# Optimization experiments

Measured on AMD Instinct MI355X. Metric: run time of the kernel, lower is better.

Reference implementation:

```python
import jax, jax.numpy as jnp
import numpy as np

N_QUBITS = 8
N_LAYERS = 4


def _apply_1q(state, U, q):
    """Apply a 2x2 gate U (shape (2,2) shared, or (B,2,2) per-sample) on qubit q.
    state: (B, 2, 2, ..., 2) with qubit q on axis q+1 (wire 0 = most significant)."""
    a = q + 1
    st = jnp.moveaxis(state, a, -1)
    shp = st.shape
    st = st.reshape(shp[0], -1, 2)  # (B, rest, 2)
    if U.ndim == 3:
        st = jnp.einsum('bij,brj->bri', U, st)
    else:
        st = jnp.einsum('ij,brj->bri', U, st)
    return jnp.moveaxis(st.reshape(shp), -1, a)


def _cnot(state, c, t):
    ac, at = c + 1, t + 1
    s0 = jnp.take(state, 0, axis=ac)
    s1 = jnp.take(state, 1, axis=ac)
    at2 = at - 1 if at > ac else at  # axis shift after removing control axis
    s1 = jnp.flip(s1, axis=at2)      # X on target where control = 1
    return jnp.stack([s0, s1], axis=ac)


def _rx(t):
    c = jnp.cos(t / 2)
    s = jnp.sin(t / 2)
    return jnp.stack([jnp.stack([c + 0j, -1j * s]),
                      jnp.stack([-1j * s, c + 0j])]).astype(jnp.complex64)


def _ry(t):
    c = jnp.cos(t / 2)
    s = jnp.sin(t / 2)
    return jnp.stack([jnp.stack([c, -s]),
                      jnp.stack([s, c])]).astype(jnp.complex64)


def _rz(t):
    return jnp.diag(jnp.stack([jnp.exp(-1j * t / 2),
                               jnp.exp(1j * t / 2)])).astype(jnp.complex64)


def _ry_batched(t):
    # t: (B,) -> (B, 2, 2)
    c = jnp.cos(t / 2)
    s = jnp.sin(t / 2)
    U = jnp.stack([jnp.stack([c, -s], axis=-1),
                   jnp.stack([s, c], axis=-1)], axis=-2)
    return U.astype(jnp.complex64)


def setup_inputs() -> dict:
    key = jax.random.key(0)
    k1, k2 = jax.random.split(key)
    B = 16384
    x = jax.random.normal(k1, (B, N_QUBITS), dtype=jnp.float32)
    weights = jax.random.normal(k2, (N_QUBITS * N_LAYERS * 3,), dtype=jnp.float32) * 0.1
    return {"x": x, "weights": weights}


def reference(x, weights):
    n, L = N_QUBITS, N_LAYERS
    B = x.shape[0]
    state = jnp.zeros((B,) + (2,) * n, dtype=jnp.complex64)
    state = state.at[(slice(None),) + (0,) * n].set(1.0)

    # angle encoding: per-sample RY on each wire
    for q in range(n):
        state = _apply_1q(state, _ry_batched(x[:, q]), q)

    idx = 0
    for _ in range(L):
        for q in range(n):
            state = _apply_1q(state, _rx(weights[idx]), q)
            state = _apply_1q(state, _ry(weights[idx + 1]), q)
            state = _apply_1q(state, _rz(weights[idx + 2]), q)
            idx += 3
        for q in range(n - 1):
            state = _cnot(state, q, q + 1)

    p = jnp.abs(state) ** 2  # (B, 2, ..., 2) float32
    outs = []
    for q in range(n):
        axes = tuple(a for a in range(1, n + 1) if a != q + 1)
        z = p.sum(axis=axes)  # (B, 2)
        outs.append(z[:, 0] - z[:, 1])
    return jnp.stack(outs, axis=-1).astype(jnp.float32)
```

## Files before the change

### kernel.cpp

```cpp
#include <hip/hip_runtime.h>


#define NGATES 32

constexpr bool selon(int l, int d) {
    return (l == 0) ? (d == 0) : (((d + l - 1) & (l - 1)) == (l - 1));
}
constexpr int lm_of(int l, int q) {
    int m = 0;
    for (int d = 0; q + d <= 7; ++d)
        if ((l & d) == d) { int qq = q + d; if (qq <= 3) m |= 1 << (3 - qq); }
    return m;
}
constexpr int rm_of(int l, int q) {
    int m = 0;
    for (int d = 0; q + d <= 7; ++d)
        if ((l & d) == d) { int qq = q + d; if (qq >= 4) m |= 1 << (7 - qq); }
    return m;
}
constexpr int slm_of(int l, int q) {
    int m = 0;
    for (int d = 0; d <= q; ++d)
        if (selon(l, d)) { int k = q - d; if (k <= 3) m |= 1 << (3 - k); }
    return m;
}
constexpr int srm_of(int l, int q) {
    int m = 0;
    for (int d = 0; d <= q; ++d)
        if (selon(l, d)) { int k = q - d; if (k >= 4) m |= 1 << (7 - k); }
    return m;
}

__device__ __forceinline__ float xsgn(float f, unsigned m) {
    return __int_as_float(__float_as_int(f) ^ (int)m);
}

template<int C>
__device__ __forceinline__ int dppmov(int x) {
    return __builtin_amdgcn_update_dpp(x, x, C, 0xF, 0xF, false);
}

template<int M>
__device__ __forceinline__ float shx(float v) {
    static_assert(M >= 1 && M <= 15, "xor mask out of range");
    int x = __float_as_int(v);
    if constexpr (M == 1)       { x = dppmov<0xB1>(x); }
    else if constexpr (M == 2)  { x = dppmov<0x4E>(x); }
    else if constexpr (M == 3)  { x = dppmov<0x1B>(x); }
    else if constexpr (M == 4)  { x = dppmov<0x1B>(x);  x = dppmov<0x141>(x); }
    else if constexpr (M == 5)  { x = dppmov<0x4E>(x);  x = dppmov<0x141>(x); }
    else if constexpr (M == 6)  { x = dppmov<0xB1>(x);  x = dppmov<0x141>(x); }
    else if constexpr (M == 7)  { x = dppmov<0x141>(x); }
    else if constexpr (M == 8)  { x = dppmov<0x128>(x); }
    else if constexpr (M == 9)  { x = dppmov<0xB1>(x);  x = dppmov<0x128>(x); }
    else if constexpr (M == 10) { x = dppmov<0x4E>(x);  x = dppmov<0x128>(x); }
    else if constexpr (M == 11) { x = dppmov<0x1B>(x);  x = dppmov<0x128>(x); }
    else if constexpr (M == 12) { x = dppmov<0x140>(x); x = dppmov<0x1B>(x);  }
    else if constexpr (M == 13) { x = dppmov<0x140>(x); x = dppmov<0x4E>(x);  }
    else if constexpr (M == 14) { x = dppmov<0x140>(x); x = dppmov<0xB1>(x);  }
    else                        { x = dppmov<0x140>(x); }
    return __int_as_float(x);
}

template<int LM, int RM, int SLM, int SRM>
__device__ __forceinline__ void apply_gate(float ar[16], float ai[16], int lane,
                                           const float4 g)
{
    unsigned sm = 0;
    if constexpr (SLM != 0)
        sm = (unsigned)((__builtin_popcount(lane & SLM) & 1) << 31);
    const float c0r = g.x, c1i = g.w;
    const float c0i0 = xsgn(g.y, sm);
    const float c1r0 = xsgn(g.z, sm);
    const float c0i1 = xsgn(g.y, sm ^ 0x80000000u);
    const float c1r1 = xsgn(g.z, sm ^ 0x80000000u);

    if constexpr (RM == 0) {
        #pragma unroll
        for (int r = 0; r < 16; ++r) {
            const bool c1 = (__builtin_popcount(r & SRM) & 1) != 0;
            const float c0i = c1 ? c0i1 : c0i0;
            const float c1r = c1 ? c1r1 : c1r0;
            const float br = shx<LM>(ar[r]);
            const float bi = shx<LM>(ai[r]);
            const float nr = c0r*ar[r] - c0i*ai[r] + c1r*br - c1i*bi;
            const float ni = c0r*ai[r] + c0i*ar[r] + c1r*bi + c1i*br;
            ar[r] = nr; ai[r] = ni;
        }
    } else {
        #pragma unroll
        for (int r = 0; r < 16; ++r) {
            const int p = r ^ RM;
            if (p < r) continue;
            float br_r, bi_r, br_p, bi_p;
            if constexpr (LM != 0) {
                br_r = shx<LM>(ar[p]); bi_r = shx<LM>(ai[p]);
                br_p = shx<LM>(ar[r]); bi_p = shx<LM>(ai[r]);
            } else {
                br_r = ar[p]; bi_r = ai[p];
                br_p = ar[r]; bi_p = ai[r];
            }
            const bool cr = (__builtin_popcount(r & SRM) & 1) != 0;
            const bool cp = (__builtin_popcount(p & SRM) & 1) != 0;
            const float c0i_r = cr ? c0i1 : c0i0, c1r_r = cr ? c1r1 : c1r0;
            const float c0i_p = cp ? c0i1 : c0i0, c1r_p = cp ? c1r1 : c1r0;
            const float nr_r = c0r*ar[r] - c0i_r*ai[r] + c1r_r*br_r - c1i*bi_r;
            const float ni_r = c0r*ai[r] + c0i_r*ar[r] + c1r_r*bi_r + c1i*br_r;
            const float nr_p = c0r*ar[p] - c0i_p*ai[p] + c1r_p*br_p - c1i*bi_p;
            const float ni_p = c0r*ai[p] + c0i_p*ar[p] + c1r_p*bi_p + c1i*br_p;
            ar[r] = nr_r; ai[r] = ni_r;
            ar[p] = nr_p; ai[p] = ni_p;
        }
    }
}

#define GATE(L, Q) apply_gate<lm_of(L,Q), rm_of(L,Q), slm_of(L,Q), srm_of(L,Q)>( \
                       ar, ai, lane, gsh4[(L)*8+(Q)])
#define LAYER(L) GATE(L,0); GATE(L,1); GATE(L,2); GATE(L,3); \
                 GATE(L,4); GATE(L,5); GATE(L,6); GATE(L,7);

__global__ __launch_bounds__(256, 4) void qsim(const float* __restrict__ x,
                                               const float* __restrict__ w,
                                               float* __restrict__ out, int B)
{
    __shared__ float4 gsh4[NGATES];

    const int tid = threadIdx.x;
    if (tid < NGATES) {
        float hx = 0.5f * w[tid*3+0];
        float hy = 0.5f * w[tid*3+1];
        float hz = 0.5f * w[tid*3+2];
        float cx = cosf(hx), sx = sinf(hx);
        float cy = cosf(hy), sy = sinf(hy);
        float cz = cosf(hz), sz = sinf(hz);
        float m00r = cy*cx,  m00i =  sy*sx;
        float m01r = -sy*cx, m01i = -cy*sx;
        gsh4[tid] = make_float4(cz*m00r + sz*m00i,
                                cz*m00i - sz*m00r,
                                cz*m01r + sz*m01i,
                                cz*m01i - sz*m01r);
    }
    __syncthreads();

    const int lane = tid & 63;
    const int il   = lane & 15;
    const int sample = blockIdx.x * 16 + (tid >> 4);
    if (sample >= B) return;

    const float4* xp = (const float4*)(x + sample * 8);
    float4 xa = xp[0], xb = xp[1];
    float xs[8] = {xa.x, xa.y, xa.z, xa.w, xb.x, xb.y, xb.z, xb.w};
    float cq[8], sq[8];
    #pragma unroll
    for (int q = 0; q < 8; ++q) {
        float h = 0.5f * xs[q];
        __sincosf(h, &sq[q], &cq[q]);
    }
    float lp = ((il & 8) ? sq[0] : cq[0]);
    lp      *= ((il & 4) ? sq[1] : cq[1]);
    lp      *= ((il & 2) ? sq[2] : cq[2]);
    lp      *= ((il & 1) ? sq[3] : cq[3]);
    float t67[4] = {cq[6]*cq[7], cq[6]*sq[7], sq[6]*cq[7], sq[6]*sq[7]};
    float a5[2]  = {cq[5], sq[5]};
    float a4[2]  = {cq[4]*lp, sq[4]*lp};
    float ar[16], ai[16];
    #pragma unroll
    for (int r = 0; r < 16; ++r) {
        ar[r] = a4[(r >> 3) & 1] * a5[(r >> 2) & 1] * t67[r & 3];
        ai[r] = 0.f;
    }

    LAYER(0)
    LAYER(1)
    LAYER(2)
    LAYER(3)

    float p[16];
    #pragma unroll
    for (int r = 0; r < 16; ++r) p[r] = ar[r]*ar[r] + ai[r]*ai[r];

    float s0[8], d0[8];
    #pragma unroll
    for (int k = 0; k < 8; ++k) { s0[k] = p[2*k] + p[2*k+1]; d0[k] = p[2*k] - p[2*k+1]; }
    float A0 = ((d0[0]+d0[1]) + (d0[2]+d0[3])) + ((d0[4]+d0[5]) + (d0[6]+d0[7]));
    float s1[4], d1[4];
    #pragma unroll
    for (int k = 0; k < 4; ++k) { s1[k] = s0[2*k] + s0[2*k+1]; d1[k] = s0[2*k] - s0[2*k+1]; }
    float A1 = (d1[0]+d1[1]) + (d1[2]+d1[3]);
    float s2[2], d2[2];
    #pragma unroll
    for (int k = 0; k < 2; ++k) { s2[k] = s1[2*k] + s1[2*k+1]; d2[k] = s1[2*k] - s1[2*k+1]; }
    float A2 = d2[0] + d2[1];
    float A3 = s2[0] - s2[1];
    float P  = s2[0] + s2[1];

    const unsigned sg1 = (unsigned)(il & 1) << 31;
    const unsigned sg2 = (unsigned)(il & 2) << 30;
    const unsigned sg4 = (unsigned)(il & 4) << 29;
    const unsigned sg8 = (unsigned)(il & 8) << 28;

    float wP = P;
    { float t = shx<1>(wP); wP = t + xsgn(wP, sg1); }
    { float t = shx<2>(wP); wP = t + xsgn(wP, sg2); }
    { float t = shx<4>(wP); wP = t + xsgn(wP, sg4); }
    { float t = shx<8>(wP); wP = t + xsgn(wP, sg8); }

    float a3 = xsgn(A3, sg8);
    a3 += shx<1>(a3); a3 += shx<2>(a3); a3 += shx<4>(a3); a3 += shx<8>(a3);
    float a2 = xsgn(A2, sg4);
    a2 += shx<1>(a2); a2 += shx<2>(a2); a2 += shx<4>(a2); a2 += shx<8>(a2);
    float a1 = xsgn(A1, sg2);
    a1 += shx<1>(a1); a1 += shx<2>(a1); a1 += shx<4>(a1); a1 += shx<8>(a1);
    float a0 = xsgn(A0, sg1);
    a0 += shx<1>(a0); a0 += shx<2>(a0); a0 += shx<4>(a0); a0 += shx<8>(a0);

    float* op = out + sample * 8;
    if (il == 8)      { op[0] = wP; op[4] = a3; }
    else if (il == 4) { op[1] = wP; op[5] = a2; }
    else if (il == 2) { op[2] = wP; op[6] = a1; }
    else if (il == 1) { op[3] = wP; op[7] = a0; }
}

extern "C" void kernel_launch(void* const* d_in, const int* in_sizes, int n_in,
                              void* d_out, int out_size, void* d_ws, size_t ws_size,
                              hipStream_t stream) {
    const float* x = (const float*)d_in[0];
    const float* w = (const float*)d_in[1];
    float* out = (float*)d_out;
    const int B = in_sizes[0] / 8;
    const int blocks = (B + 15) / 16;
    qsim<<<blocks, 256, 0, stream>>>(x, w, out, B);
}
```

Baseline: 92.70 us.

## Pack complex amplitudes into float2 and use packed FMA with ds_swizzle shuffles

Stores each complex amplitude as a two-float vector and computes each gate update with four packed v_pk_mul/v_pk_fma instructions in inline asm, where the scalar version needed separate real and imaginary FMAs. The intent is to roughly halve VALU instruction count for the gate math. Lane-xor masks that needed two DPP moves now use a single ds_swizzle, which trades VALU work for LDS-pipe latency. The inline asm may also limit compiler scheduling and add register-pair move overhead.

```diff
diff --git a/kernel.cpp b/kernel.cpp
--- a/kernel.cpp
+++ b/kernel.cpp
@@ -2,6 +2,10 @@
 
 
 #define NGATES 32
+
+typedef float v2f __attribute__((ext_vector_type(2)));
+
+__device__ __forceinline__ v2f mk2(float a, float b) { v2f t; t.x = a; t.y = b; return t; }
 
 constexpr bool selon(int l, int d) {
     return (l == 0) ? (d == 0) : (((d + l - 1) & (l - 1)) == (l - 1));
@@ -34,88 +38,90 @@
 __device__ __forceinline__ float xsgn(float f, unsigned m) {
     return __int_as_float(__float_as_int(f) ^ (int)m);
 }
+
 
 template<int C>
 __device__ __forceinline__ int dppmov(int x) {
     return __builtin_amdgcn_update_dpp(x, x, C, 0xF, 0xF, false);
 }
-
 template<int M>
-__device__ __forceinline__ float shx(float v) {
-    static_assert(M >= 1 && M <= 15, "xor mask out of range");
+__device__ __forceinline__ float shx_dpp(float v) {
     int x = __float_as_int(v);
     if constexpr (M == 1)       { x = dppmov<0xB1>(x); }
     else if constexpr (M == 2)  { x = dppmov<0x4E>(x); }
     else if constexpr (M == 3)  { x = dppmov<0x1B>(x); }
-    else if constexpr (M == 4)  { x = dppmov<0x1B>(x);  x = dppmov<0x141>(x); }
-    else if constexpr (M == 5)  { x = dppmov<0x4E>(x);  x = dppmov<0x141>(x); }
-    else if constexpr (M == 6)  { x = dppmov<0xB1>(x);  x = dppmov<0x141>(x); }
     else if constexpr (M == 7)  { x = dppmov<0x141>(x); }
     else if constexpr (M == 8)  { x = dppmov<0x128>(x); }
-    else if constexpr (M == 9)  { x = dppmov<0xB1>(x);  x = dppmov<0x128>(x); }
-    else if constexpr (M == 10) { x = dppmov<0x4E>(x);  x = dppmov<0x128>(x); }
-    else if constexpr (M == 11) { x = dppmov<0x1B>(x);  x = dppmov<0x128>(x); }
-    else if constexpr (M == 12) { x = dppmov<0x140>(x); x = dppmov<0x1B>(x);  }
-    else if constexpr (M == 13) { x = dppmov<0x140>(x); x = dppmov<0x4E>(x);  }
-    else if constexpr (M == 14) { x = dppmov<0x140>(x); x = dppmov<0xB1>(x);  }
     else                        { x = dppmov<0x140>(x); }
     return __int_as_float(x);
 }
+template<int M>
+__device__ __forceinline__ float shx_ds(float v) {
+    return __int_as_float(__builtin_amdgcn_ds_swizzle(__float_as_int(v), (M << 10) | 0x1F));
+}
+constexpr bool sgl(int M) {
+    return M == 1 || M == 2 || M == 3 || M == 7 || M == 8 || M == 15;
+}
+template<int M>
+__device__ __forceinline__ float shxm(float v) {
+    if constexpr (sgl(M)) return shx_dpp<M>(v);
+    else                  return shx_ds<M>(v);
+}
+
+__device__ __forceinline__ v2f cplx4(v2f K0, v2f K1, v2f A, v2f B) {
+    v2f n;
+    asm("v_pk_mul_f32 %0, %1, %2 op_sel:[0,0] op_sel_hi:[0,1]\n\t"
+        "v_pk_fma_f32 %0, %1, %2, %0 op_sel:[1,1,0] op_sel_hi:[1,0,1] neg_lo:[1,0,0]\n\t"
+        "v_pk_fma_f32 %0, %3, %4, %0 op_sel:[0,0,0] op_sel_hi:[0,1,1]\n\t"
+        "v_pk_fma_f32 %0, %3, %4, %0 op_sel:[1,1,0] op_sel_hi:[1,0,1] neg_lo:[1,0,0]"
+        : "=&v"(n)
+        : "v"(K0), "v"(A), "v"(K1), "v"(B));
+    return n;
+}
 
 template<int LM, int RM, int SLM, int SRM>
-__device__ __forceinline__ void apply_gate(float ar[16], float ai[16], int lane,
-                                           const float4 g)
+__device__ __forceinline__ void apply_gate(v2f A[16], int lane, const float4 g)
 {
     unsigned sm = 0;
     if constexpr (SLM != 0)
         sm = (unsigned)((__builtin_popcount(lane & SLM) & 1) << 31);
-    const float c0r = g.x, c1i = g.w;
-    const float c0i0 = xsgn(g.y, sm);
-    const float c1r0 = xsgn(g.z, sm);
-    const float c0i1 = xsgn(g.y, sm ^ 0x80000000u);
-    const float c1r1 = xsgn(g.z, sm ^ 0x80000000u);
+    v2f K0[2], K1[2];
+    K0[0] = mk2(g.x, xsgn(g.y, sm));
+    K0[1] = mk2(g.x, xsgn(g.y, sm ^ 0x80000000u));
+    K1[0] = mk2(xsgn(g.z, sm), g.w);
+    K1[1] = mk2(xsgn(g.z, sm ^ 0x80000000u), g.w);
 
     if constexpr (RM == 0) {
         #pragma unroll
         for (int r = 0; r < 16; ++r) {
-            const bool c1 = (__builtin_popcount(r & SRM) & 1) != 0;
-            const float c0i = c1 ? c0i1 : c0i0;
-            const float c1r = c1 ? c1r1 : c1r0;
-            const float br = shx<LM>(ar[r]);
-            const float bi = shx<LM>(ai[r]);
-            const float nr = c0r*ar[r] - c0i*ai[r] + c1r*br - c1i*bi;
-            const float ni = c0r*ai[r] + c0i*ar[r] + c1r*bi + c1i*br;
-            ar[r] = nr; ai[r] = ni;
+            const int v = __builtin_popcount(r & SRM) & 1;
+            v2f B = mk2(shxm<LM>(A[r].x), shxm<LM>(A[r].y));
+            A[r] = cplx4(K0[v], K1[v], A[r], B);
         }
     } else {
         #pragma unroll
         for (int r = 0; r < 16; ++r) {
             const int p = r ^ RM;
             if (p < r) continue;
-            float br_r, bi_r, br_p, bi_p;
+            v2f Br, Bp;
             if constexpr (LM != 0) {
-                br_r = shx<LM>(ar[p]); bi_r = shx<LM>(ai[p]);
-                br_p = shx<LM>(ar[r]); bi_p = shx<LM>(ai[r]);
+                Br = mk2(shxm<LM>(A[p].x), shxm<LM>(A[p].y));
+                Bp = mk2(shxm<LM>(A[r].x), shxm<LM>(A[r].y));
             } else {
-                br_r = ar[p]; bi_r = ai[p];
-                br_p = ar[r]; bi_p = ai[r];
+                Br = A[p];
+                Bp = A[r];
             }
-            const bool cr = (__builtin_popcount(r & SRM) & 1) != 0;
-            const bool cp = (__builtin_popcount(p & SRM) & 1) != 0;
-            const float c0i_r = cr ? c0i1 : c0i0, c1r_r = cr ? c1r1 : c1r0;
-            const float c0i_p = cp ? c0i1 : c0i0, c1r_p = cp ? c1r1 : c1r0;
-            const float nr_r = c0r*ar[r] - c0i_r*ai[r] + c1r_r*br_r - c1i*bi_r;
-            const float ni_r = c0r*ai[r] + c0i_r*ar[r] + c1r_r*bi_r + c1i*br_r;
-            const float nr_p = c0r*ar[p] - c0i_p*ai[p] + c1r_p*br_p - c1i*bi_p;
-            const float ni_p = c0r*ai[p] + c0i_p*ar[p] + c1r_p*bi_p + c1i*br_p;
-            ar[r] = nr_r; ai[r] = ni_r;
-            ar[p] = nr_p; ai[p] = ni_p;
+            const int vr = __builtin_popcount(r & SRM) & 1;
+            const int vp = __builtin_popcount(p & SRM) & 1;
+            v2f nr = cplx4(K0[vr], K1[vr], A[r], Br);
+            v2f np = cplx4(K0[vp], K1[vp], A[p], Bp);
+            A[r] = nr; A[p] = np;
         }
     }
 }
 
 #define GATE(L, Q) apply_gate<lm_of(L,Q), rm_of(L,Q), slm_of(L,Q), srm_of(L,Q)>( \
-                       ar, ai, lane, gsh4[(L)*8+(Q)])
+                       A, lane, gsh4[(L)*8+(Q)])
 #define LAYER(L) GATE(L,0); GATE(L,1); GATE(L,2); GATE(L,3); \
                  GATE(L,4); GATE(L,5); GATE(L,6); GATE(L,7);
 
@@ -163,12 +169,10 @@
     float t67[4] = {cq[6]*cq[7], cq[6]*sq[7], sq[6]*cq[7], sq[6]*sq[7]};
     float a5[2]  = {cq[5], sq[5]};
     float a4[2]  = {cq[4]*lp, sq[4]*lp};
-    float ar[16], ai[16];
-    #pragma unroll
-    for (int r = 0; r < 16; ++r) {
-        ar[r] = a4[(r >> 3) & 1] * a5[(r >> 2) & 1] * t67[r & 3];
-        ai[r] = 0.f;
-    }
+    v2f A[16];
+    #pragma unroll
+    for (int r = 0; r < 16; ++r)
+        A[r] = mk2(a4[(r >> 3) & 1] * a5[(r >> 2) & 1] * t67[r & 3], 0.f);
 
     LAYER(0)
     LAYER(1)
@@ -177,7 +181,7 @@
 
     float p[16];
     #pragma unroll
-    for (int r = 0; r < 16; ++r) p[r] = ar[r]*ar[r] + ai[r]*ai[r];
+    for (int r = 0; r < 16; ++r) p[r] = A[r].x*A[r].x + A[r].y*A[r].y;
 
     float s0[8], d0[8];
     #pragma unroll
@@ -200,19 +204,19 @@
     const unsigned sg8 = (unsigned)(il & 8) << 28;
 
     float wP = P;
-    { float t = shx<1>(wP); wP = t + xsgn(wP, sg1); }
-    { float t = shx<2>(wP); wP = t + xsgn(wP, sg2); }
-    { float t = shx<4>(wP); wP = t + xsgn(wP, sg4); }
-    { float t = shx<8>(wP); wP = t + xsgn(wP, sg8); }
+    { float t = shxm<1>(wP); wP = t + xsgn(wP, sg1); }
+    { float t = shxm<2>(wP); wP = t + xsgn(wP, sg2); }
+    { float t = shxm<4>(wP); wP = t + xsgn(wP, sg4); }
+    { float t = shxm<8>(wP); wP = t + xsgn(wP, sg8); }
 
     float a3 = xsgn(A3, sg8);
-    a3 += shx<1>(a3); a3 += shx<2>(a3); a3 += shx<4>(a3); a3 += shx<8>(a3);
+    a3 += shxm<1>(a3); a3 += shxm<2>(a3); a3 += shxm<4>(a3); a3 += shxm<8>(a3);
     float a2 = xsgn(A2, sg4);
-    a2 += shx<1>(a2); a2 += shx<2>(a2); a2 += shx<4>(a2); a2 += shx<8>(a2);
+    a2 += shxm<1>(a2); a2 += shxm<2>(a2); a2 += shxm<4>(a2); a2 += shxm<8>(a2);
     float a1 = xsgn(A1, sg2);
-    a1 += shx<1>(a1); a1 += shx<2>(a1); a1 += shx<4>(a1); a1 += shx<8>(a1);
+    a1 += shxm<1>(a1); a1 += shxm<2>(a1); a1 += shxm<4>(a1); a1 += shxm<8>(a1);
     float a0 = xsgn(A0, sg1);
-    a0 += shx<1>(a0); a0 += shx<2>(a0); a0 += shx<4>(a0); a0 += shx<8>(a0);
+    a0 += shxm<1>(a0); a0 += shxm<2>(a0); a0 += shxm<4>(a0); a0 += shxm<8>(a0);
 
     float* op = out + sample * 8;
     if (il == 8)      { op[0] = wP; op[4] = a3; }
```

Result: faster. 78.55 us (-15.3%).

## Fold first rotation layer into product-state init and use ds_swizzle for two-step shuffles

Applied to the files above, without the earlier changes.

The first layer's single-qubit rotations are folded into the initial product state: each qubit's encoding RY is combined with its layer-0 gate analytically, and the 16 amplitudes per lane are built as complex products. This removes a full LAYER(0) pass of lane shuffles and complex FMAs, since before the first CNOT ladder the state is still a product state. Lane xor-shuffles that needed two DPP moves now use a single ds_swizzle instead, trading two DPP ops for one LDS-crossbar op with higher latency. The folding assumes layer 0 consists only of 1-qubit gates before its CNOTs, and it relies on the LAYER macro still applying layer 0's CNOTs, which is not visible here.

```diff
diff --git a/kernel.cpp b/kernel.cpp
--- a/kernel.cpp
+++ b/kernel.cpp
@@ -39,27 +39,28 @@
 __device__ __forceinline__ int dppmov(int x) {
     return __builtin_amdgcn_update_dpp(x, x, C, 0xF, 0xF, false);
 }
-
 template<int M>
-__device__ __forceinline__ float shx(float v) {
-    static_assert(M >= 1 && M <= 15, "xor mask out of range");
+__device__ __forceinline__ float shx_dpp(float v) {
     int x = __float_as_int(v);
     if constexpr (M == 1)       { x = dppmov<0xB1>(x); }
     else if constexpr (M == 2)  { x = dppmov<0x4E>(x); }
     else if constexpr (M == 3)  { x = dppmov<0x1B>(x); }
-    else if constexpr (M == 4)  { x = dppmov<0x1B>(x);  x = dppmov<0x141>(x); }
-    else if constexpr (M == 5)  { x = dppmov<0x4E>(x);  x = dppmov<0x141>(x); }
-    else if constexpr (M == 6)  { x = dppmov<0xB1>(x);  x = dppmov<0x141>(x); }
     else if constexpr (M == 7)  { x = dppmov<0x141>(x); }
     else if constexpr (M == 8)  { x = dppmov<0x128>(x); }
-    else if constexpr (M == 9)  { x = dppmov<0xB1>(x);  x = dppmov<0x128>(x); }
-    else if constexpr (M == 10) { x = dppmov<0x4E>(x);  x = dppmov<0x128>(x); }
-    else if constexpr (M == 11) { x = dppmov<0x1B>(x);  x = dppmov<0x128>(x); }
-    else if constexpr (M == 12) { x = dppmov<0x140>(x); x = dppmov<0x1B>(x);  }
-    else if constexpr (M == 13) { x = dppmov<0x140>(x); x = dppmov<0x4E>(x);  }
-    else if constexpr (M == 14) { x = dppmov<0x140>(x); x = dppmov<0xB1>(x);  }
     else                        { x = dppmov<0x140>(x); }
     return __int_as_float(x);
+}
+template<int M>
+__device__ __forceinline__ float shx_ds(float v) {
+    return __int_as_float(__builtin_amdgcn_ds_swizzle(__float_as_int(v), (M << 10) | 0x1F));
+}
+constexpr bool sgl(int M) {
+    return M == 1 || M == 2 || M == 3 || M == 7 || M == 8 || M == 15;
+}
+template<int M>
+__device__ __forceinline__ float shxm(float v) {
+    if constexpr (sgl(M)) return shx_dpp<M>(v);
+    else                  return shx_ds<M>(v);
 }
 
 template<int LM, int RM, int SLM, int SRM>
@@ -81,8 +82,8 @@
             const bool c1 = (__builtin_popcount(r & SRM) & 1) != 0;
             const float c0i = c1 ? c0i1 : c0i0;
             const float c1r = c1 ? c1r1 : c1r0;
-            const float br = shx<LM>(ar[r]);
-            const float bi = shx<LM>(ai[r]);
+            const float br = shxm<LM>(ar[r]);
+            const float bi = shxm<LM>(ai[r]);
             const float nr = c0r*ar[r] - c0i*ai[r] + c1r*br - c1i*bi;
             const float ni = c0r*ai[r] + c0i*ar[r] + c1r*bi + c1i*br;
             ar[r] = nr; ai[r] = ni;
@@ -94,8 +95,8 @@
             if (p < r) continue;
             float br_r, bi_r, br_p, bi_p;
             if constexpr (LM != 0) {
-                br_r = shx<LM>(ar[p]); bi_r = shx<LM>(ai[p]);
-                br_p = shx<LM>(ar[r]); bi_p = shx<LM>(ai[r]);
+                br_r = shxm<LM>(ar[p]); bi_r = shxm<LM>(ai[p]);
+                br_p = shxm<LM>(ar[r]); bi_p = shxm<LM>(ai[r]);
             } else {
                 br_r = ar[p]; bi_r = ai[p];
                 br_p = ar[r]; bi_p = ai[r];
@@ -150,27 +151,63 @@
     const float4* xp = (const float4*)(x + sample * 8);
     float4 xa = xp[0], xb = xp[1];
     float xs[8] = {xa.x, xa.y, xa.z, xa.w, xb.x, xb.y, xb.z, xb.w};
-    float cq[8], sq[8];
+    float arf[8], aif[8], brf[8], bif[8];
     #pragma unroll
     for (int q = 0; q < 8; ++q) {
-        float h = 0.5f * xs[q];
-        __sincosf(h, &sq[q], &cq[q]);
-    }
-    float lp = ((il & 8) ? sq[0] : cq[0]);
-    lp      *= ((il & 4) ? sq[1] : cq[1]);
-    lp      *= ((il & 2) ? sq[2] : cq[2]);
-    lp      *= ((il & 1) ? sq[3] : cq[3]);
-    float t67[4] = {cq[6]*cq[7], cq[6]*sq[7], sq[6]*cq[7], sq[6]*sq[7]};
-    float a5[2]  = {cq[5], sq[5]};
-    float a4[2]  = {cq[4]*lp, sq[4]*lp};
+        float c, s;
+        __sincosf(0.5f * xs[q], &s, &c);
+        const float4 g = gsh4[q];
+        arf[q] = g.x*c + g.z*s;
+        aif[q] = g.y*c + g.w*s;
+        brf[q] = g.x*s - g.z*c;
+        bif[q] = g.w*c - g.y*s;
+    }
+    float Fr = (il & 8) ? brf[0] : arf[0];
+    float Fi = (il & 8) ? bif[0] : aif[0];
+    #pragma unroll
+    for (int q = 1; q < 4; ++q) {
+        const int bit = il & (8 >> q);
+        const float gr = bit ? brf[q] : arf[q];
+        const float gi = bit ? bif[q] : aif[q];
+        const float nr = Fr*gr - Fi*gi;
+        const float ni = Fr*gi + Fi*gr;
+        Fr = nr; Fi = ni;
+    }
+    float t67r[4], t67i[4];
+    #pragma unroll
+    for (int b6 = 0; b6 < 2; ++b6)
+        #pragma unroll
+        for (int b7 = 0; b7 < 2; ++b7) {
+            const float x6r = b6 ? brf[6] : arf[6], x6i = b6 ? bif[6] : aif[6];
+            const float x7r = b7 ? brf[7] : arf[7], x7i = b7 ? bif[7] : aif[7];
+            t67r[b6*2+b7] = x6r*x7r - x6i*x7i;
+            t67i[b6*2+b7] = x6r*x7i + x6i*x7r;
+        }
+    float v57r[8], v57i[8];
+    #pragma unroll
+    for (int b5 = 0; b5 < 2; ++b5) {
+        const float x5r = b5 ? brf[5] : arf[5], x5i = b5 ? bif[5] : aif[5];
+        #pragma unroll
+        for (int k = 0; k < 4; ++k) {
+            v57r[b5*4+k] = x5r*t67r[k] - x5i*t67i[k];
+            v57i[b5*4+k] = x5r*t67i[k] + x5i*t67r[k];
+        }
+    }
+    float b4r[2], b4i[2];
+    #pragma unroll
+    for (int b4 = 0; b4 < 2; ++b4) {
+        const float x4r = b4 ? brf[4] : arf[4], x4i = b4 ? bif[4] : aif[4];
+        b4r[b4] = x4r*Fr - x4i*Fi;
+        b4i[b4] = x4r*Fi + x4i*Fr;
+    }
     float ar[16], ai[16];
     #pragma unroll
     for (int r = 0; r < 16; ++r) {
-        ar[r] = a4[(r >> 3) & 1] * a5[(r >> 2) & 1] * t67[r & 3];
-        ai[r] = 0.f;
-    }
-
-    LAYER(0)
+        const int hi = (r >> 3) & 1, lo = r & 7;
+        ar[r] = b4r[hi]*v57r[lo] - b4i[hi]*v57i[lo];
+        ai[r] = b4r[hi]*v57i[lo] + b4i[hi]*v57r[lo];
+    }
+
     LAYER(1)
     LAYER(2)
     LAYER(3)
@@ -200,19 +237,19 @@
     const unsigned sg8 = (unsigned)(il & 8) << 28;
 
     float wP = P;
-    { float t = shx<1>(wP); wP = t + xsgn(wP, sg1); }
-    { float t = shx<2>(wP); wP = t + xsgn(wP, sg2); }
-    { float t = shx<4>(wP); wP = t + xsgn(wP, sg4); }
-    { float t = shx<8>(wP); wP = t + xsgn(wP, sg8); }
+    { float t = shxm<1>(wP); wP = t + xsgn(wP, sg1); }
+    { float t = shxm<2>(wP); wP = t + xsgn(wP, sg2); }
+    { float t = shxm<4>(wP); wP = t + xsgn(wP, sg4); }
+    { float t = shxm<8>(wP); wP = t + xsgn(wP, sg8); }
 
     float a3 = xsgn(A3, sg8);
-    a3 += shx<1>(a3); a3 += shx<2>(a3); a3 += shx<4>(a3); a3 += shx<8>(a3);
+    a3 += shxm<1>(a3); a3 += shxm<2>(a3); a3 += shxm<4>(a3); a3 += shxm<8>(a3);
     float a2 = xsgn(A2, sg4);
-    a2 += shx<1>(a2); a2 += shx<2>(a2); a2 += shx<4>(a2); a2 += shx<8>(a2);
+    a2 += shxm<1>(a2); a2 += shxm<2>(a2); a2 += shxm<4>(a2); a2 += shxm<8>(a2);
     float a1 = xsgn(A1, sg2);
-    a1 += shx<1>(a1); a1 += shx<2>(a1); a1 += shx<4>(a1); a1 += shx<8>(a1);
+    a1 += shxm<1>(a1); a1 += shxm<2>(a1); a1 += shxm<4>(a1); a1 += shxm<8>(a1);
     float a0 = xsgn(A0, sg1);
-    a0 += shx<1>(a0); a0 += shx<2>(a0); a0 += shx<4>(a0); a0 += shx<8>(a0);
+    a0 += shxm<1>(a0); a0 += shxm<2>(a0); a0 += shxm<4>(a0); a0 += shxm<8>(a0);
 
     float* op = out + sample * 8;
     if (il == 8)      { op[0] = wP; op[4] = a3; }
```

After: 81.69 us. -11.9%, faster.
